# Kernel optimization log

Measured on AMD Instinct MI355X. Metric: run time of the kernel, lower is better.

## Reference

```python
import jax, jax.numpy as jnp
import numpy as np

DIMS = 1024
HEAD = 16
HEAD_DIM = DIMS // HEAD
B, S = 1, 2048


def setup_inputs() -> dict:
    key = jax.random.key(0)
    ks = jax.random.split(key, 8)
    init = lambda k, shape: (jax.random.normal(k, shape, dtype=jnp.float32) * 0.02)
    x = jax.random.normal(ks[0], (B, S, DIMS), dtype=jnp.float32)
    mask = jnp.zeros((S, S), dtype=jnp.float32)
    Wq = init(ks[1], (DIMS, DIMS)); bq = jnp.zeros((DIMS,), jnp.float32)
    Wk = init(ks[2], (DIMS, DIMS))  # k projection has no bias
    Wv = init(ks[3], (DIMS, DIMS)); bv = jnp.zeros((DIMS,), jnp.float32)
    Wo = init(ks[4], (DIMS, DIMS)); bo = jnp.zeros((DIMS,), jnp.float32)
    Zfactor = jnp.asarray(1e-05, dtype=jnp.float32)
    inv_freq = 1.0 / (10000.0 ** (jnp.arange(0, HEAD_DIM, 2, dtype=jnp.float32) / HEAD_DIM))
    return {"x": x, "mask": mask, "Wq": Wq, "bq": bq, "Wk": Wk, "Wv": Wv,
            "bv": bv, "Wo": Wo, "bo": bo, "Zfactor": Zfactor, "inv_freq": inv_freq}


def _apply_rotary(u, cos, sin):
    # u: [B,H,S,hd]; cos/sin: [S,hd/2]. Pairs are consecutive (view_as_complex).
    a = u[..., 0::2]
    b = u[..., 1::2]
    ra = a * cos - b * sin
    rb = a * sin + b * cos
    return jnp.stack([ra, rb], axis=-1).reshape(u.shape)


def reference(x, mask, Wq, bq, Wk, Wv, bv, Wo, bo, Zfactor, inv_freq):
    Bx, Sx, D = x.shape
    H, hd = HEAD, D // HEAD
    q = x @ Wq.T + bq
    k = x @ Wk.T          # no bias on k
    v = x @ Wv.T + bv
    # [B,S,D] -> [B,H,S,hd]
    split = lambda u: u.reshape(Bx, Sx, H, hd).transpose(0, 2, 1, 3)
    q, k, v = split(q), split(k), split(v)
    # RoPE frequencies: t outer inv_freq -> [S, hd/2]
    t = jnp.arange(Sx, dtype=jnp.float32)
    freqs = t[:, None] * inv_freq[None, :]
    cos, sin = jnp.cos(freqs), jnp.sin(freqs)
    q = _apply_rotary(q, cos, sin)
    k = _apply_rotary(k, cos, sin)
    scale = hd ** (-0.25)
    qk = jnp.einsum('bhqd,bhkd->bhqk', q * scale, k * scale)
    # custom zscale: pad positions (token id 0 taken as first feature of k) get tiny factor
    token_ids = k[..., 0]  # [B,H,Sk]
    zfactor = jnp.clip(jax.nn.softplus(Zfactor), 1e-05, 0.0001)
    zscale = jnp.where(token_ids == 0.0, zfactor, 1.0)  # [B,H,Sk]
    qk = qk + mask[None, None, :Sx, :Sx] * zscale[:, :, None, :]
    qk = qk * zscale[:, :, None, :]
    w = jax.nn.softmax(qk, axis=-1)
    wv = jnp.einsum('bhqk,bhkd->bhqd', w, v)
    wv = wv.transpose(0, 2, 1, 3).reshape(Bx, Sx, D)
    out = wv @ Wo.T + bo
    return out, qk
```

## Files before the change

kernel.cpp:

```cpp
#include <hip/hip_runtime.h>
#include <hip/hip_bf16.h>

#define SEQ 2048
#define DIM 1024
#define NH  16
#define HD  64
#define SPLIT 4
#define KCOLS (SEQ / SPLIT)
#define KVBLK 128
#define CREF 10.0f

typedef __bf16 bf16_t;
typedef __bf16 bf16x4 __attribute__((ext_vector_type(4)));
typedef __bf16 bf16x8 __attribute__((ext_vector_type(8)));
typedef float  f32x4  __attribute__((ext_vector_type(4)));

#define MFMA16(a,b,c) __builtin_amdgcn_mfma_f32_16x16x32_bf16((a),(b),(c),0,0,0)

__device__ __forceinline__ void gload_lds16(const void* g, void* l) {
    __builtin_amdgcn_global_load_lds(
        (const __attribute__((address_space(1))) unsigned int*)g,
        (__attribute__((address_space(3))) unsigned int*)l, 16, 0, 0);
}

__global__ __launch_bounds__(256) void k_tables(const float* __restrict__ invf,
                                                float* __restrict__ cosT,
                                                float* __restrict__ sinT) {
    int id = blockIdx.x * 256 + threadIdx.x;
    int t = id >> 5, i = id & 31;
    float f = (float)t * invf[i];
    cosT[id] = cosf(f);
    sinT[id] = sinf(f);
}

__global__ void k_zeroflag(int* __restrict__ flag) { flag[0] = 0; }

__global__ __launch_bounds__(256) void k_maskchk(const float* __restrict__ mask,
                                                 int* __restrict__ flag) {
    int id = blockIdx.x * 256 + threadIdx.x;
    f32x4 v = *(const f32x4*)(mask + (size_t)id * 4);
    bool nz = (v[0] != 0.f) | (v[1] != 0.f) | (v[2] != 0.f) | (v[3] != 0.f);
    if (__any(nz) && (threadIdx.x & 63) == 0) atomicOr(flag, 1);
}

__global__ __launch_bounds__(256) void k_cvt_all(const float* __restrict__ x,
                                                 const float* __restrict__ Wq,
                                                 const float* __restrict__ Wk,
                                                 const float* __restrict__ Wv,
                                                 const float* __restrict__ Wo,
                                                 bf16_t* __restrict__ Xb,
                                                 bf16_t* __restrict__ Wqkvb,
                                                 bf16_t* __restrict__ Wob) {
    int id = blockIdx.x * 256 + threadIdx.x;
    const float* src;
    bf16_t* dst;
    int off;
    if (id < 524288)       { src = x;  dst = Xb;              off = id; }
    else if (id < 786432)  { src = Wq; dst = Wqkvb;           off = id - 524288; }
    else if (id < 1048576) { src = Wk; dst = Wqkvb + 1048576; off = id - 786432; }
    else if (id < 1310720) { src = Wv; dst = Wqkvb + 2097152; off = id - 1048576; }
    else                   { src = Wo; dst = Wob;             off = id - 1310720; }
    float4 v = ((const float4*)src)[off];
    bf16x4 o;
    o[0] = (bf16_t)v.x; o[1] = (bf16_t)v.y; o[2] = (bf16_t)v.z; o[3] = (bf16_t)v.w;
    ((bf16x4*)dst)[off] = o;
}

__global__ __launch_bounds__(256) void k_biasqkv(const float* __restrict__ bq,
                                                 const float* __restrict__ bv,
                                                 float* __restrict__ bqkv) {
    int n = blockIdx.x * 256 + threadIdx.x;
    bqkv[n] = (n < 1024) ? bq[n] : ((n < 2048) ? 0.0f : bv[n - 2048]);
}

__global__ __launch_bounds__(256) void gemm128(const bf16_t* __restrict__ A,
                                               const bf16_t* __restrict__ W,
                                               const float* __restrict__ bias,
                                               bf16_t* __restrict__ outBf,
                                               float* __restrict__ outF,
                                               int N, int K) {
    __shared__ __align__(16) bf16_t As[2][128 * 32];
    __shared__ __align__(16) bf16_t Bs[2][128 * 32];
    int tid = threadIdx.x, wid = tid >> 6, lane = tid & 63;
    int lrow = lane >> 4, lcol = lane & 15;
    int wr = wid >> 1, wc = wid & 1;

    int orig = blockIdx.y * gridDim.x + blockIdx.x;
    int cpx = (gridDim.x * gridDim.y) >> 3;
    int swzb = (orig & 7) * cpx + (orig >> 3);
    int m0 = (swzb % gridDim.x) * 128;
    int n0 = (swzb / gridDim.x) * 128;

    int sr = wid * 32 + (lane >> 2);
    int sc = (lane & 3) * 8;
    const bf16_t* Ag = A + (size_t)(m0 + sr) * K + sc;
    const bf16_t* Wg = W + (size_t)(n0 + sr) * K + sc;

    f32x4 acc[4][4] = {};

#define STAGE(buf, k0) do { \
        gload_lds16(Ag + (k0),          &As[buf][wid * 1024]);       \
        gload_lds16(Ag + 16 * K + (k0), &As[buf][wid * 1024 + 512]); \
        gload_lds16(Wg + (k0),          &Bs[buf][wid * 1024]);       \
        gload_lds16(Wg + 16 * K + (k0), &Bs[buf][wid * 1024 + 512]); \
    } while (0)

    STAGE(0, 0);
    __syncthreads();
    int buf = 0;
    for (int k0 = 0; k0 < K; k0 += 32) {
        if (k0 + 32 < K) STAGE(buf ^ 1, k0 + 32);
        bf16x8 af[4], bfr[4];
#pragma unroll
        for (int mi = 0; mi < 4; mi++)
            af[mi] = *(const bf16x8*)&As[buf][(wr * 64 + mi * 16 + lcol) * 32 + lrow * 8];
#pragma unroll
        for (int ni = 0; ni < 4; ni++)
            bfr[ni] = *(const bf16x8*)&Bs[buf][(wc * 64 + ni * 16 + lcol) * 32 + lrow * 8];
#pragma unroll
        for (int mi = 0; mi < 4; mi++)
#pragma unroll
            for (int ni = 0; ni < 4; ni++)
                acc[mi][ni] = MFMA16(af[mi], bfr[ni], acc[mi][ni]);
        __syncthreads();
        buf ^= 1;
    }
#undef STAGE
#pragma unroll
    for (int ni = 0; ni < 4; ni++) {
        int col = n0 + wc * 64 + ni * 16 + lcol;
        float bb = bias ? bias[col] : 0.0f;
#pragma unroll
        for (int mi = 0; mi < 4; mi++)
#pragma unroll
            for (int j = 0; j < 4; j++) {
                int row = m0 + wr * 64 + mi * 16 + lrow * 4 + j;
                float v = acc[mi][ni][j] + bb;
                if (outBf) outBf[(size_t)row * N + col] = (bf16_t)v;
                else       outF [(size_t)row * N + col] = v;
            }
    }
}

__global__ __launch_bounds__(256) void k_rope(const bf16_t* __restrict__ QKV,
                                              const float* __restrict__ cosT,
                                              const float* __restrict__ sinT,
                                              const float* __restrict__ Zf,
                                              bf16_t* __restrict__ Qh,
                                              bf16_t* __restrict__ Kh,
                                              float* __restrict__ zsq) {
    int id = blockIdx.x * 256 + threadIdx.x;
    int s = id >> 9, pp = id & 511;
    int h = pp >> 5, i = pp & 31;
    float c  = cosT[s * 32 + i];
    float sn = sinT[s * 32 + i];
    const float scale = 0.3535533905932738f;
    size_t qb = (size_t)s * 3072 + h * HD + 2 * i;
    size_t kb = qb + 1024;
    size_t ob = ((size_t)h * SEQ + s) * HD + 2 * i;

    float qa = (float)QKV[qb], qbv = (float)QKV[qb + 1];
    Qh[ob]     = (bf16_t)((qa * c - qbv * sn) * scale);
    Qh[ob + 1] = (bf16_t)((qa * sn + qbv * c) * scale);

    float k0a = (float)QKV[(size_t)s * 3072 + 1024 + h * HD];
    float k0b = (float)QKV[(size_t)s * 3072 + 1024 + h * HD + 1];
    float ra0 = k0a * cosT[s * 32] - k0b * sinT[s * 32];
    float z = Zf[0];
    float zfac = fminf(fmaxf(log1pf(__expf(z)), 1e-5f), 1e-4f);
    float zs = (ra0 == 0.0f) ? zfac : 1.0f;

    float ka = (float)QKV[kb], kbv = (float)QKV[kb + 1];
    float ra = ka * c - kbv * sn;
    float rb = ka * sn + kbv * c;
    Kh[ob]     = (bf16_t)(ra * scale * zs);
    Kh[ob + 1] = (bf16_t)(rb * scale * zs);
    if (i == 0) zsq[h * SEQ + s] = zs * zs;
}

__global__ __launch_bounds__(256) void k_transpose(const bf16_t* __restrict__ QKV,
                                                   bf16_t* __restrict__ Vt) {
    __shared__ bf16_t tile[64][66];
    int t = threadIdx.x;
    int c = t & 63, r4 = t >> 6;
    int s0 = blockIdx.x * 64, d0 = blockIdx.y * 64;
#pragma unroll
    for (int i = 0; i < 16; i++) {
        int r = i * 4 + r4;
        tile[r][c] = QKV[(size_t)(s0 + r) * 3072 + 2048 + d0 + c];
    }
    __syncthreads();
#pragma unroll
    for (int i = 0; i < 16; i++) {
        int r = i * 4 + r4;
        Vt[(size_t)(d0 + r) * SEQ + s0 + c] = tile[c][r];
    }
}

__global__ __launch_bounds__(256) void k_attn(const bf16_t* __restrict__ Qh,
                                              const bf16_t* __restrict__ Kh,
                                              const bf16_t* __restrict__ Vt,
                                              const float* __restrict__ mask,
                                              const float* __restrict__ zsq,
                                              const int* __restrict__ mflag,
                                              float* __restrict__ qk_out,
                                              bf16_t* __restrict__ Opart,
                                              float* __restrict__ Lpart) {
    __shared__ __align__(16) char Ks[2][16384];
    __shared__ __align__(16) char Vs[2][16384];
    __shared__ __align__(16) char Plds[4][4096];
    int tid = threadIdx.x, wid = tid >> 6, lane = tid & 63;
    int lrow = lane >> 4, lcol = lane & 15;

    int orig = blockIdx.x;
    int s = (orig & 7) * 256 + (orig >> 3);
    int h = s >> 7;
    int rem = s & 127;
    int qblk = rem & 31, sp = rem >> 5;

    int q0 = qblk * 64 + wid * 16;
    int kbase = sp * KCOLS;
    int mz = mflag[0];

    bf16x8 aq[2];
    {
        const bf16_t* qb = Qh + ((size_t)h * SEQ + q0 + lcol) * HD + lrow * 8;
        aq[0] = *(const bf16x8*)qb;
        aq[1] = *(const bf16x8*)(qb + 32);
    }

    float l = 0.f;
    f32x4 acc[4] = {};
    char* wl = &Plds[wid][0];
    float* qkbase = qk_out + (size_t)h * SEQ * SEQ;
    const float* mrow = mask + (size_t)(q0 + lcol) * SEQ;
    const bf16_t* khead = Kh + (size_t)h * SEQ * HD;
    const bf16_t* vthead = Vt + (size_t)h * HD * SEQ;
    const float*  zrow  = zsq + h * SEQ;
    int swzP = (lcol & 7) << 4;
    int l7 = lcol & 7;

    int so[4], krk[4], ksk[4], vrv[4], vsv[4];
#pragma unroll
    for (int i = 0; i < 4; i++) {
        int o = wid * 4096 + i * 1024 + lane * 16;
        so[i] = wid * 4096 + i * 1024;
        krk[i] = o >> 7;
        ksk[i] = ((o >> 4) & 7) ^ (krk[i] & 7);
        vrv[i] = o >> 8;
        int cv = (o >> 4) & 15;
        vsv[i] = (cv & 8) | ((cv & 7) ^ (vrv[i] & 7));
    }

#define STAGEKV(b, kc0) do { \
        _Pragma("unroll") \
        for (int i = 0; i < 4; i++) { \
            gload_lds16(khead + (size_t)((kc0) + krk[i]) * HD + ksk[i] * 8, Ks[b] + so[i]); \
            gload_lds16(vthead + (size_t)vrv[i] * SEQ + (kc0) + vsv[i] * 8,  Vs[b] + so[i]); \
        } \
    } while (0)

    STAGEKV(0, kbase);
    __syncthreads();
    int buf = 0;

    for (int kc = kbase; kc < kbase + KCOLS; kc += KVBLK) {
        if (kc + KVBLK < kbase + KCOLS) STAGEKV(buf ^ 1, kc + KVBLK);

        float p[8][4];
#pragma unroll
        for (int ct = 0; ct < 8; ct++) {
            int row = ct * 16 + lcol;
            int a0 = row * 128 + ((lrow ^ l7) << 4);
            bf16x8 k0 = *(const bf16x8*)(Ks[buf] + a0);
            bf16x8 k1 = *(const bf16x8*)(Ks[buf] + (a0 ^ 64));
            f32x4 cacc = {};
            cacc = MFMA16(k0, aq[0], cacc);
            cacc = MFMA16(k1, aq[1], cacc);
#pragma unroll
            for (int j = 0; j < 4; j++) p[ct][j] = cacc[j];
        }
        if (mz) {
#pragma unroll
            for (int ct = 0; ct < 8; ct++) {
                int k4 = kc + ct * 16 + lrow * 4;
                f32x4 mv = *(const f32x4*)(mrow + k4);
                f32x4 zv = *(const f32x4*)(zrow + k4);
#pragma unroll
                for (int j = 0; j < 4; j++)
                    p[ct][j] = fmaf(mv[j], zv[j], p[ct][j]);
            }
        }
#pragma unroll
        for (int ct = 0; ct < 8; ct++) {
            bf16x4 pk;
#pragma unroll
            for (int j = 0; j < 4; j++) {
                float e = __expf(p[ct][j] - CREF);
                l += e;
                pk[j] = (bf16_t)e;
            }
            int addr = (lcol << 8) + ((ct * 16 + lrow * 4) << 1);
            *(bf16x4*)(wl + (addr ^ swzP)) = pk;
        }
        bf16x8 pa[4];
#pragma unroll
        for (int ks = 0; ks < 4; ks++) {
            int addr = (lcol << 8) + (ks << 6) + (lrow << 4);
            pa[ks] = *(const bf16x8*)(wl + (addr ^ swzP));
        }
        __builtin_amdgcn_s_setprio(1);
#pragma unroll
        for (int ks = 0; ks < 4; ks++) {
            int c = ks * 4 + lrow;
            int cs = (c & 8) | ((c & 7) ^ l7);
#pragma unroll
            for (int ng = 0; ng < 4; ng++) {
                int a = (ng * 16 + lcol) * 256 + (cs << 4);
                bf16x8 bv = *(const bf16x8*)(Vs[buf] + a);
                acc[ng] = MFMA16(bv, pa[ks], acc[ng]);
            }
        }
        __builtin_amdgcn_s_setprio(0);
#pragma unroll
        for (int ct = 0; ct < 8; ct++) {
            int k4 = kc + ct * 16 + lrow * 4;
            f32x4 ov;
#pragma unroll
            for (int j = 0; j < 4; j++) ov[j] = p[ct][j];
            *(f32x4*)(qkbase + (size_t)(q0 + lcol) * SEQ + k4) = ov;
        }
        __syncthreads();
        buf ^= 1;
    }
#undef STAGEKV
#pragma unroll
    for (int ng = 0; ng < 4; ng++) {
        bf16x4 o4;
#pragma unroll
        for (int j = 0; j < 4; j++) o4[j] = (bf16_t)acc[ng][j];
        size_t idx = ((size_t)(h * SEQ + q0 + lcol) * SPLIT + sp) * HD + ng * 16 + lrow * 4;
        *(bf16x4*)(Opart + idx) = o4;
    }
    l += __shfl_xor(l, 16);
    l += __shfl_xor(l, 32);
    if (lane < 16) {
        Lpart[((size_t)h * SEQ + q0 + lane) * SPLIT + sp] = l;
    }
}

__global__ __launch_bounds__(256) void k_combine(const bf16_t* __restrict__ Opart,
                                                 const float* __restrict__ Lpart,
                                                 bf16_t* __restrict__ wv) {
    int gid = blockIdx.x * 256 + threadIdx.x;
    int rowIdx = gid >> 6, d = gid & 63;
    const float* lp = Lpart + (size_t)rowIdx * SPLIT;
    float L = 0.f, O = 0.f;
    const bf16_t* ob = Opart + (size_t)rowIdx * SPLIT * HD + d;
#pragma unroll
    for (int s = 0; s < SPLIT; s++) {
        L += lp[s];
        O += (float)ob[(size_t)s * HD];
    }
    int h = rowIdx >> 11, row = rowIdx & (SEQ - 1);
    wv[(size_t)row * DIM + h * HD + d] = (bf16_t)(O / L);
}

extern "C" void kernel_launch(void* const* d_in, const int* in_sizes, int n_in,
                              void* d_out, int out_size, void* d_ws, size_t ws_size,
                              hipStream_t stream) {
    const float* x    = (const float*)d_in[0];
    const float* mask = (const float*)d_in[1];
    const float* Wq   = (const float*)d_in[2];
    const float* bq   = (const float*)d_in[3];
    const float* Wk   = (const float*)d_in[4];
    const float* Wv   = (const float*)d_in[5];
    const float* bv   = (const float*)d_in[6];
    const float* Wo   = (const float*)d_in[7];
    const float* bo   = (const float*)d_in[8];
    const float* Zf   = (const float*)d_in[9];
    const float* invf = (const float*)d_in[10];

    char* ws = (char*)d_ws;
    size_t off = 0;
    auto alloc = [&](size_t bytes) -> char* {
        char* p = ws + off;
        off += (bytes + 255) & ~(size_t)255;
        return p;
    };
    float*  cosT  = (float*)alloc(65536 * 4);
    float*  sinT  = (float*)alloc(65536 * 4);
    bf16_t* Xb    = (bf16_t*)alloc((size_t)SEQ * DIM * 2);
    bf16_t* Wqkvb = (bf16_t*)alloc((size_t)3 * DIM * DIM * 2);
    bf16_t* Wob   = (bf16_t*)alloc((size_t)DIM * DIM * 2);
    float*  bqkv  = (float*)alloc(3072 * 4);
    bf16_t* QKV   = (bf16_t*)alloc((size_t)SEQ * 3 * DIM * 2);
    bf16_t* Qhp   = (bf16_t*)alloc((size_t)SEQ * DIM * 2);
    bf16_t* Khp   = (bf16_t*)alloc((size_t)SEQ * DIM * 2);
    bf16_t* Vt    = (bf16_t*)alloc((size_t)DIM * SEQ * 2);
    float*  zsq   = (float*)alloc((size_t)NH * SEQ * 4);
    bf16_t* Opart = (bf16_t*)alloc((size_t)NH * SEQ * SPLIT * HD * 2);
    float*  Lpart = (float*)alloc((size_t)NH * SEQ * SPLIT * 4);
    bf16_t* WVb   = (bf16_t*)alloc((size_t)SEQ * DIM * 2);
    int*    mflag = (int*)alloc(256);

    float* outp = (float*)d_out;
    float* qkp  = outp + (size_t)SEQ * DIM;

    k_zeroflag<<<1, 1, 0, stream>>>(mflag);
    k_maskchk<<<(SEQ * SEQ / 4) / 256, 256, 0, stream>>>(mask, mflag);
    k_tables<<<256, 256, 0, stream>>>(invf, cosT, sinT);
    k_cvt_all<<<6144, 256, 0, stream>>>(x, Wq, Wk, Wv, Wo, Xb, Wqkvb, Wob);
    k_biasqkv<<<12, 256, 0, stream>>>(bq, bv, bqkv);

    gemm128<<<dim3(SEQ / 128, 3072 / 128), 256, 0, stream>>>(Xb, Wqkvb, bqkv, QKV, nullptr, 3072, DIM);

    k_rope<<<(SEQ * 512) / 256, 256, 0, stream>>>(QKV, cosT, sinT, Zf, Qhp, Khp, zsq);
    k_transpose<<<dim3(SEQ / 64, NH), 256, 0, stream>>>(QKV, Vt);

    k_attn<<<NH * (SEQ / 64) * SPLIT, 256, 0, stream>>>(Qhp, Khp, Vt, mask, zsq, mflag,
                                                        qkp, Opart, Lpart);
    k_combine<<<(NH * SEQ * HD) / 256, 256, 0, stream>>>(Opart, Lpart, WVb);

    gemm128<<<dim3(SEQ / 128, DIM / 128), 256, 0, stream>>>(WVb, Wob, bo, nullptr, outp, DIM, DIM);
}
```

Measured before the change: 158.8 us.

## Single-buffer K/V staging in attention and fold flag reset into table kernel

```diff
diff --git a/kernel.cpp b/kernel.cpp
--- a/kernel.cpp
+++ b/kernel.cpp
@@ -25,15 +25,15 @@
 
 __global__ __launch_bounds__(256) void k_tables(const float* __restrict__ invf,
                                                 float* __restrict__ cosT,
-                                                float* __restrict__ sinT) {
+                                                float* __restrict__ sinT,
+                                                int* __restrict__ flag) {
     int id = blockIdx.x * 256 + threadIdx.x;
+    if (id == 0) flag[0] = 0;
     int t = id >> 5, i = id & 31;
     float f = (float)t * invf[i];
     cosT[id] = cosf(f);
     sinT[id] = sinf(f);
 }
-
-__global__ void k_zeroflag(int* __restrict__ flag) { flag[0] = 0; }
 
 __global__ __launch_bounds__(256) void k_maskchk(const float* __restrict__ mask,
                                                  int* __restrict__ flag) {
@@ -206,8 +206,8 @@
                                               float* __restrict__ qk_out,
                                               bf16_t* __restrict__ Opart,
                                               float* __restrict__ Lpart) {
-    __shared__ __align__(16) char Ks[2][16384];
-    __shared__ __align__(16) char Vs[2][16384];
+    __shared__ __align__(16) char Ks[16384];
+    __shared__ __align__(16) char Vs[16384];
     __shared__ __align__(16) char Plds[4][4096];
     int tid = threadIdx.x, wid = tid >> 6, lane = tid & 63;
     int lrow = lane >> 4, lcol = lane & 15;
@@ -252,28 +252,21 @@
         vsv[i] = (cv & 8) | ((cv & 7) ^ (vrv[i] & 7));
     }
 
-#define STAGEKV(b, kc0) do { \
-        _Pragma("unroll") \
-        for (int i = 0; i < 4; i++) { \
-            gload_lds16(khead + (size_t)((kc0) + krk[i]) * HD + ksk[i] * 8, Ks[b] + so[i]); \
-            gload_lds16(vthead + (size_t)vrv[i] * SEQ + (kc0) + vsv[i] * 8,  Vs[b] + so[i]); \
-        } \
-    } while (0)
-
-    STAGEKV(0, kbase);
-    __syncthreads();
-    int buf = 0;
-
     for (int kc = kbase; kc < kbase + KCOLS; kc += KVBLK) {
-        if (kc + KVBLK < kbase + KCOLS) STAGEKV(buf ^ 1, kc + KVBLK);
+#pragma unroll
+        for (int i = 0; i < 4; i++) {
+            gload_lds16(khead + (size_t)(kc + krk[i]) * HD + ksk[i] * 8, Ks + so[i]);
+            gload_lds16(vthead + (size_t)vrv[i] * SEQ + kc + vsv[i] * 8,  Vs + so[i]);
+        }
+        __syncthreads();
 
         float p[8][4];
 #pragma unroll
         for (int ct = 0; ct < 8; ct++) {
             int row = ct * 16 + lcol;
             int a0 = row * 128 + ((lrow ^ l7) << 4);
-            bf16x8 k0 = *(const bf16x8*)(Ks[buf] + a0);
-            bf16x8 k1 = *(const bf16x8*)(Ks[buf] + (a0 ^ 64));
+            bf16x8 k0 = *(const bf16x8*)(Ks + a0);
+            bf16x8 k1 = *(const bf16x8*)(Ks + (a0 ^ 64));
             f32x4 cacc = {};
             cacc = MFMA16(k0, aq[0], cacc);
             cacc = MFMA16(k1, aq[1], cacc);
@@ -317,7 +310,7 @@
 #pragma unroll
             for (int ng = 0; ng < 4; ng++) {
                 int a = (ng * 16 + lcol) * 256 + (cs << 4);
-                bf16x8 bv = *(const bf16x8*)(Vs[buf] + a);
+                bf16x8 bv = *(const bf16x8*)(Vs + a);
                 acc[ng] = MFMA16(bv, pa[ks], acc[ng]);
             }
         }
@@ -331,9 +324,7 @@
             *(f32x4*)(qkbase + (size_t)(q0 + lcol) * SEQ + k4) = ov;
         }
         __syncthreads();
-        buf ^= 1;
-    }
-#undef STAGEKV
+    }
 #pragma unroll
     for (int ng = 0; ng < 4; ng++) {
         bf16x4 o4;
@@ -407,9 +398,8 @@
     float* outp = (float*)d_out;
     float* qkp  = outp + (size_t)SEQ * DIM;
 
-    k_zeroflag<<<1, 1, 0, stream>>>(mflag);
+    k_tables<<<256, 256, 0, stream>>>(invf, cosT, sinT, mflag);
     k_maskchk<<<(SEQ * SEQ / 4) / 256, 256, 0, stream>>>(mask, mflag);
-    k_tables<<<256, 256, 0, stream>>>(invf, cosT, sinT);
     k_cvt_all<<<6144, 256, 0, stream>>>(x, Wq, Wk, Wv, Wo, Xb, Wqkvb, Wob);
     k_biasqkv<<<12, 256, 0, stream>>>(bq, bv, bqkv);
 
```

Measured after the change: 154.4 us. 1.03x faster.
